# Kernel optimization log

Measured on AMD Instinct MI355X. Metric: run time of the kernel, lower is better.

Reference implementation:

```python
import jax, jax.numpy as jnp
import numpy as np

N = 100000   # num nodes
E = 1200000  # num edges
D = 64       # embedding dim
K = 3        # propagation hops (alpha has K+1 entries)


def setup_inputs() -> dict:
    key = jax.random.key(0)
    k1, k2, k3 = jax.random.split(key, 3)
    edge_index = jax.random.randint(k1, (2, E), 0, N, dtype=jnp.int64)
    weight = jax.random.normal(k2, (N, D), dtype=jnp.float32)
    alpha = jax.random.uniform(k3, (K + 1,), dtype=jnp.float32)
    return {"edge_index": edge_index, "weight": weight, "alpha": alpha}


def reference(edge_index, weight, alpha):
    row = edge_index[0]  # source j
    col = edge_index[1]  # target i
    # symmetric normalization: in-degree over col, deg^-1/2 with inf -> 0
    deg = jax.ops.segment_sum(jnp.ones((E,), dtype=weight.dtype), col, num_segments=N)
    dinv = jnp.where(deg == 0, 0.0, deg ** -0.5)
    edge_w = dinv[row] * dinv[col]  # [E]

    out = weight * alpha[0]
    x = weight
    for k in range(1, K + 1):
        # gather-scale-scatter propagation hop
        msg = edge_w[:, None] * x[row]                      # [E, D]
        x = jax.ops.segment_sum(msg, col, num_segments=N)   # [N, D]
        out = out + x * alpha[k]

    # per-edge link scores: dot(out[src], out[dst])
    return jnp.sum(out[row] * out[col], axis=-1)  # [E]
```

## Files before the change

### kernel.cpp

```cpp
#include <hip/hip_runtime.h>
#include <hip/hip_bf16.h>

#define GN 100000
#define GE 1200000
#define GD 64
#define NG 256
#define CPG 391
#define CAP 6144


__global__ void detect_kernel(const void* __restrict__ w,
                              const void* __restrict__ edge,
                              int* __restrict__ flags, int* __restrict__ gcount) {
    __shared__ int s_badw, s_edgenz;
    if (threadIdx.x == 0) { s_badw = 0; s_edgenz = 0; }
    gcount[threadIdx.x] = 0;
    __syncthreads();
    const unsigned short* wh = (const unsigned short*)w;
    const unsigned int*   ei = (const unsigned int*)edge;
    int badw = 0, edgenz = 0;
    for (int i = threadIdx.x; i < 4096; i += 256) {
        unsigned int bits = ((unsigned int)wh[i]) << 16;
        float v = __uint_as_float(bits);
        if (!(fabsf(v) <= 100.0f)) badw = 1;
        if ((i & 1) == 1 && ei[i] != 0u) edgenz = 1;
    }
    if (badw)   atomicOr(&s_badw, 1);
    if (edgenz) atomicOr(&s_edgenz, 1);
    __syncthreads();
    if (threadIdx.x == 0) {
        flags[0] = s_badw ? 0 : 1;
        flags[1] = s_edgenz ? 0 : 1;
    }
}

__device__ __forceinline__ int ld_row(const int* __restrict__ edge, int e, int e64) {
    return e64 ? edge[2 * (size_t)e] : edge[e];
}
__device__ __forceinline__ int ld_col(const int* __restrict__ edge, int e, int e64) {
    return e64 ? edge[2 * ((size_t)GE + (size_t)e)] : edge[(size_t)GE + (size_t)e];
}
__device__ __forceinline__ float ld_f(const void* __restrict__ p, size_t i, int bf16f) {
    if (bf16f) return __bfloat162float(((const __hip_bfloat16*)p)[i]);
    return ((const float*)p)[i];
}

__device__ __forceinline__ float bf_lo(unsigned u) { return __uint_as_float(u << 16); }
__device__ __forceinline__ float bf_hi(unsigned u) { return __uint_as_float(u & 0xFFFF0000u); }
__device__ __forceinline__ unsigned bf16bits(float f) {
    __hip_bfloat16 h = __float2bfloat16(f);
    unsigned short s;
    __builtin_memcpy(&s, &h, 2);
    return (unsigned)s;
}

__global__ void p1init_kernel(const int* __restrict__ edge, const int* __restrict__ flags,
                              int* __restrict__ gcount, unsigned* __restrict__ bucket,
                              int E, int chunk,
                              const void* __restrict__ w, const void* __restrict__ alpha,
                              __hip_bfloat16* __restrict__ X,
                              __hip_bfloat16* __restrict__ OUT, int nd) {
    if (blockIdx.x < NG) {
        __shared__ int cnt[NG];
        __shared__ int base[NG];
        int t = threadIdx.x;
        int e64 = flags[1];
        cnt[t] = 0;
        __syncthreads();
        int lo = blockIdx.x * chunk;
        int hiE = min(lo + chunk, E);
        for (int e = lo + t; e < hiE; e += 256) {
            int c = ld_col(edge, e, e64);
            int r = ld_row(edge, e, e64);
            if ((unsigned)c < (unsigned)GN && (unsigned)r < (unsigned)GN)
                atomicAdd(&cnt[c / CPG], 1);
        }
        __syncthreads();
        int cv = cnt[t];
        base[t] = (cv > 0) ? atomicAdd(&gcount[t], cv) : 0;
        __syncthreads();
        cnt[t] = 0;
        __syncthreads();
        for (int e = lo + t; e < hiE; e += 256) {
            int c = ld_col(edge, e, e64);
            int r = ld_row(edge, e, e64);
            if ((unsigned)c < (unsigned)GN && (unsigned)r < (unsigned)GN) {
                int g = c / CPG;
                int idx = base[g] + atomicAdd(&cnt[g], 1);
                if (idx < CAP)
                    bucket[(size_t)g * CAP + idx] = ((unsigned)(c - g * CPG) << 17) | (unsigned)r;
            }
        }
    } else {
        int bid = blockIdx.x - NG;
        int i = 4 * (bid * 256 + (int)threadIdx.x);
        int wbf = flags[0];
        if (i < nd) {
            float a0 = ld_f(alpha, 0, wbf);
            float v0 = ld_f(w, i + 0, wbf);
            float v1 = ld_f(w, i + 1, wbf);
            float v2 = ld_f(w, i + 2, wbf);
            float v3 = ld_f(w, i + 3, wbf);
            uint2 xq;
            xq.x = (bf16bits(v1) << 16) | bf16bits(v0);
            xq.y = (bf16bits(v3) << 16) | bf16bits(v2);
            *(uint2*)(X + i) = xq;
            uint2 oq;
            oq.x = (bf16bits(a0 * v1) << 16) | bf16bits(a0 * v0);
            oq.y = (bf16bits(a0 * v3) << 16) | bf16bits(a0 * v2);
            *(uint2*)(OUT + i) = oq;
        }
    }
}

__global__ void p2_kernel(const unsigned* __restrict__ bucket, const int* __restrict__ gcount,
                          int* __restrict__ rowptr, float* __restrict__ dinv,
                          int* __restrict__ csr) {
    int g = blockIdx.x;
    int t = threadIdx.x;
    __shared__ int gs[NG];
    __shared__ int hist[512];
    __shared__ int s[512];
    int gv = gcount[t]; if (gv > CAP) gv = CAP;
    gs[t] = gv;
    hist[t] = 0; hist[t + 256] = 0;
    __syncthreads();
    for (int off = 1; off < NG; off <<= 1) {
        int u = (t >= off) ? gs[t - off] : 0;
        __syncthreads();
        gs[t] += u;
        __syncthreads();
    }
    int mg = gcount[g]; if (mg > CAP) mg = CAP;
    int gb = gs[g] - mg;
    int m = mg;
    const unsigned* bk = bucket + (size_t)g * CAP;
    for (int idx = t; idx < m; idx += 256)
        atomicAdd(&hist[bk[idx] >> 17], 1);
    __syncthreads();
    int h0 = hist[t], h1 = hist[t + 256];
    s[t] = h0; s[t + 256] = h1;
    __syncthreads();
    for (int off = 1; off < 512; off <<= 1) {
        int v0 = (t >= off) ? s[t - off] : 0;
        int v1 = (t + 256 >= off) ? s[t + 256 - off] : 0;
        __syncthreads();
        s[t] += v0; s[t + 256] += v1;
        __syncthreads();
    }
    int col0 = g * CPG + t;
    int col1 = col0 + 256;
    if (col0 < GN) {
        rowptr[col0] = gb + s[t];
        dinv[col0] = (h0 > 0) ? rsqrtf((float)h0) : 0.0f;
    }
    if (t + 256 < CPG && col1 < GN) {
        rowptr[col1] = gb + s[t + 256];
        dinv[col1] = (h1 > 0) ? rsqrtf((float)h1) : 0.0f;
    }
    __syncthreads();
    hist[t] = s[t] - h0;
    hist[t + 256] = s[t + 256] - h1;
    __syncthreads();
    for (int idx = t; idx < m; idx += 256) {
        unsigned u = bk[idx];
        int cl = u >> 17;
        int r  = (int)(u & 0x1FFFFu);
        int pos = gb + atomicAdd(&hist[cl], 1);
        csr[pos] = r;
    }
}

__global__ void gather_kernel(const __hip_bfloat16* __restrict__ X,
                              __hip_bfloat16* __restrict__ Y,
                              __hip_bfloat16* __restrict__ OUT,
                              const int* __restrict__ rowptr, const int* __restrict__ csr,
                              const float* __restrict__ dinv,
                              const void* __restrict__ alpha, const int* __restrict__ flags,
                              int k, int store_y, int N) {
    int t = blockIdx.x * blockDim.x + threadIdx.x;
    int node = __builtin_amdgcn_readfirstlane(t >> 6);
    if (node >= N) return;
    int lane = t & 63;
    int h = lane >> 4;
    int i = lane & 15;
    int beg = node ? rowptr[node - 1] : 0;
    int end = rowptr[node];
    float dc = dinv[node];
    float a = ld_f(alpha, k, flags[0]);
    size_t obase = (size_t)node * GD + 4 * i;
    uint2 uo = *(const uint2*)(OUT + obase);
    float f0 = 0.0f, f1 = 0.0f, f2 = 0.0f, f3 = 0.0f;
    for (int j = beg; j < end; j += 16) {
        int i0 = j + 0 + h;  int i1 = j + 4 + h;
        int i2 = j + 8 + h;  int i3 = j + 12 + h;
        int last = end - 1;
        int r0 = csr[min(i0, last)];
        int r1 = csr[min(i1, last)];
        int r2 = csr[min(i2, last)];
        int r3 = csr[min(i3, last)];
        float w0 = (i0 < end) ? dinv[r0] : 0.0f;
        float w1 = (i1 < end) ? dinv[r1] : 0.0f;
        float w2 = (i2 < end) ? dinv[r2] : 0.0f;
        float w3 = (i3 < end) ? dinv[r3] : 0.0f;
        uint2 u0 = *(const uint2*)(X + (size_t)r0 * GD + 4 * i);
        uint2 u1 = *(const uint2*)(X + (size_t)r1 * GD + 4 * i);
        uint2 u2 = *(const uint2*)(X + (size_t)r2 * GD + 4 * i);
        uint2 u3 = *(const uint2*)(X + (size_t)r3 * GD + 4 * i);
        f0 = fmaf(w0, bf_lo(u0.x), f0); f1 = fmaf(w0, bf_hi(u0.x), f1);
        f2 = fmaf(w0, bf_lo(u0.y), f2); f3 = fmaf(w0, bf_hi(u0.y), f3);
        f0 = fmaf(w1, bf_lo(u1.x), f0); f1 = fmaf(w1, bf_hi(u1.x), f1);
        f2 = fmaf(w1, bf_lo(u1.y), f2); f3 = fmaf(w1, bf_hi(u1.y), f3);
        f0 = fmaf(w2, bf_lo(u2.x), f0); f1 = fmaf(w2, bf_hi(u2.x), f1);
        f2 = fmaf(w2, bf_lo(u2.y), f2); f3 = fmaf(w2, bf_hi(u2.y), f3);
        f0 = fmaf(w3, bf_lo(u3.x), f0); f1 = fmaf(w3, bf_hi(u3.x), f1);
        f2 = fmaf(w3, bf_lo(u3.y), f2); f3 = fmaf(w3, bf_hi(u3.y), f3);
    }
    f0 += __shfl_xor(f0, 16, 64); f0 += __shfl_xor(f0, 32, 64);
    f1 += __shfl_xor(f1, 16, 64); f1 += __shfl_xor(f1, 32, 64);
    f2 += __shfl_xor(f2, 16, 64); f2 += __shfl_xor(f2, 32, 64);
    f3 += __shfl_xor(f3, 16, 64); f3 += __shfl_xor(f3, 32, 64);
    f0 *= dc; f1 *= dc; f2 *= dc; f3 *= dc;
    if (h == 0) {
        if (store_y) {
            uint2 p;
            p.x = (bf16bits(f1) << 16) | bf16bits(f0);
            p.y = (bf16bits(f3) << 16) | bf16bits(f2);
            *(uint2*)(Y + obase) = p;
        }
        float o0 = fmaf(a, f0, bf_lo(uo.x));
        float o1 = fmaf(a, f1, bf_hi(uo.x));
        float o2 = fmaf(a, f2, bf_lo(uo.y));
        float o3 = fmaf(a, f3, bf_hi(uo.y));
        uint2 q;
        q.x = (bf16bits(o1) << 16) | bf16bits(o0);
        q.y = (bf16bits(o3) << 16) | bf16bits(o2);
        *(uint2*)(OUT + obase) = q;
    }
}

__device__ __forceinline__ float dot2_bf16(unsigned ua, unsigned ub) {
    return fmaf(bf_lo(ua), bf_lo(ub), bf_hi(ua) * bf_hi(ub));
}

__global__ void dot_kernel(const __hip_bfloat16* __restrict__ OUT,
                           const int* __restrict__ edge, const int* __restrict__ flags,
                           void* __restrict__ res, int E) {
    int t = blockIdx.x * blockDim.x + threadIdx.x;
    int e = t >> 2;
    int sub = t & 3;
    if (e >= E) return;
    int e64 = flags[1];
    int wbf = flags[0];
    int r = ld_row(edge, e, e64);
    int c = ld_col(edge, e, e64);
    float p = 0.0f;
    if ((unsigned)r < (unsigned)GN && (unsigned)c < (unsigned)GN) {
        const uint4* pa = (const uint4*)(OUT + (size_t)r * GD + sub * 16);
        const uint4* pb = (const uint4*)(OUT + (size_t)c * GD + sub * 16);
        uint4 a0 = pa[0], a1 = pa[1];
        uint4 b0 = pb[0], b1 = pb[1];
        p = ((dot2_bf16(a0.x, b0.x) + dot2_bf16(a0.y, b0.y)) +
             (dot2_bf16(a0.z, b0.z) + dot2_bf16(a0.w, b0.w))) +
            ((dot2_bf16(a1.x, b1.x) + dot2_bf16(a1.y, b1.y)) +
             (dot2_bf16(a1.z, b1.z) + dot2_bf16(a1.w, b1.w)));
    }
    p += __shfl_down(p, 2, 4);
    p += __shfl_down(p, 1, 4);
    if (sub == 0) {
        if (wbf) ((__hip_bfloat16*)res)[e] = __float2bfloat16(p);
        else     ((float*)res)[e] = p;
    }
}

extern "C" void kernel_launch(void* const* d_in, const int* in_sizes, int n_in,
                              void* d_out, int out_size, void* d_ws, size_t ws_size,
                              hipStream_t stream) {
    const int E = GE, N = GN, ND = GN * GD;

    const void* edge   = d_in[0];
    const void* weight = d_in[1];
    const void* alpha  = d_in[2];

    char* ws = (char*)d_ws;
    int*      flags     = (int*)ws;      ws += 256;
    int*      gcount    = (int*)ws;      ws += 1024;
    float*    dinv      = (float*)ws;    ws += (((size_t)N * 4 + 255) / 256) * 256;
    int*      rowptr    = (int*)ws;      ws += (((size_t)N * 4 + 255) / 256) * 256;
    unsigned* bucket    = (unsigned*)ws; ws += (size_t)NG * CAP * 4;
    int*      csr       = (int*)ws;      ws += (size_t)E * 4;
    __hip_bfloat16* X   = (__hip_bfloat16*)ws; ws += (size_t)ND * 2;
    __hip_bfloat16* Y   = (__hip_bfloat16*)ws; ws += (size_t)ND * 2;
    __hip_bfloat16* OUT = (__hip_bfloat16*)ws; ws += (size_t)ND * 2;

    const int B = 256;

    detect_kernel<<<1, 256, 0, stream>>>(weight, edge, flags, gcount);

    {
        const int chunk = (E + NG - 1) / NG;
        const int initBlocks = (ND / 4 + B - 1) / B;
        p1init_kernel<<<NG + initBlocks, B, 0, stream>>>(
            (const int*)edge, flags, gcount, bucket, E, chunk,
            weight, alpha, X, OUT, ND);
    }
    p2_kernel<<<NG, 256, 0, stream>>>(bucket, gcount, rowptr, dinv, csr);

    const int ggrid = (int)(((size_t)N * 64 + B - 1) / B);
    gather_kernel<<<ggrid, B, 0, stream>>>(X, Y, OUT, rowptr, csr, dinv, alpha, flags, 1, 1, N);
    gather_kernel<<<ggrid, B, 0, stream>>>(Y, X, OUT, rowptr, csr, dinv, alpha, flags, 2, 1, N);
    gather_kernel<<<ggrid, B, 0, stream>>>(X, Y, OUT, rowptr, csr, dinv, alpha, flags, 3, 0, N);

    dot_kernel<<<(int)(((size_t)E * 4 + B - 1) / B), B, 0, stream>>>(OUT, (const int*)edge, flags, d_out, E);
}
```

Before: 275.2 us.

## Fuse three gather hops and edge dot into one cooperative persistent kernel

Replaces the three per-hop gather launches and the dot-product launch with a single cooperative kernel. Persistent waves loop over nodes and edges, and each phase is separated by a grid-wide barrier. This is meant to remove launch gaps and tail effects between kernels, at the cost of grid.sync overhead and occupancy capped by the co-residency requirement. The grid size comes from an occupancy query that assumes 256 compute units.

```diff
diff --git a/kernel.cpp b/kernel.cpp
--- a/kernel.cpp
+++ b/kernel.cpp
@@ -1,5 +1,8 @@
 #include <hip/hip_runtime.h>
 #include <hip/hip_bf16.h>
+#include <hip/hip_cooperative_groups.h>
+
+namespace cg = cooperative_groups;
 
 #define GN 100000
 #define GE 1200000
@@ -171,23 +174,17 @@
     }
 }
 
-__global__ void gather_kernel(const __hip_bfloat16* __restrict__ X,
-                              __hip_bfloat16* __restrict__ Y,
-                              __hip_bfloat16* __restrict__ OUT,
-                              const int* __restrict__ rowptr, const int* __restrict__ csr,
-                              const float* __restrict__ dinv,
-                              const void* __restrict__ alpha, const int* __restrict__ flags,
-                              int k, int store_y, int N) {
-    int t = blockIdx.x * blockDim.x + threadIdx.x;
-    int node = __builtin_amdgcn_readfirstlane(t >> 6);
-    if (node >= N) return;
-    int lane = t & 63;
+__device__ __forceinline__ void gather_node(
+        const __hip_bfloat16* __restrict__ X, __hip_bfloat16* __restrict__ Y,
+        __hip_bfloat16* __restrict__ OUT,
+        const int* __restrict__ rowptr, const int* __restrict__ csr,
+        const float* __restrict__ dinv, float a, int store_y,
+        int node, int lane) {
     int h = lane >> 4;
     int i = lane & 15;
     int beg = node ? rowptr[node - 1] : 0;
     int end = rowptr[node];
     float dc = dinv[node];
-    float a = ld_f(alpha, k, flags[0]);
     size_t obase = (size_t)node * GD + 4 * i;
     uint2 uo = *(const uint2*)(OUT + obase);
     float f0 = 0.0f, f1 = 0.0f, f2 = 0.0f, f3 = 0.0f;
@@ -243,33 +240,69 @@
     return fmaf(bf_lo(ua), bf_lo(ub), bf_hi(ua) * bf_hi(ub));
 }
 
-__global__ void dot_kernel(const __hip_bfloat16* __restrict__ OUT,
-                           const int* __restrict__ edge, const int* __restrict__ flags,
-                           void* __restrict__ res, int E) {
-    int t = blockIdx.x * blockDim.x + threadIdx.x;
-    int e = t >> 2;
-    int sub = t & 3;
-    if (e >= E) return;
+__global__ void coop_kernel(__hip_bfloat16* __restrict__ X,
+                            __hip_bfloat16* __restrict__ Y,
+                            __hip_bfloat16* __restrict__ OUT,
+                            const int* __restrict__ rowptr, const int* __restrict__ csr,
+                            const float* __restrict__ dinv,
+                            const void* __restrict__ alpha, const int* __restrict__ flags,
+                            const int* __restrict__ edge, void* __restrict__ res,
+                            int N, int E) {
+    cg::grid_group grid = cg::this_grid();
+    int lane = threadIdx.x & 63;
+    int wslot = blockIdx.x * 4 + (threadIdx.x >> 6);
+    int totalWaves = gridDim.x * 4;
+    int wbf = flags[0];
     int e64 = flags[1];
-    int wbf = flags[0];
-    int r = ld_row(edge, e, e64);
-    int c = ld_col(edge, e, e64);
-    float p = 0.0f;
-    if ((unsigned)r < (unsigned)GN && (unsigned)c < (unsigned)GN) {
-        const uint4* pa = (const uint4*)(OUT + (size_t)r * GD + sub * 16);
-        const uint4* pb = (const uint4*)(OUT + (size_t)c * GD + sub * 16);
-        uint4 a0 = pa[0], a1 = pa[1];
-        uint4 b0 = pb[0], b1 = pb[1];
-        p = ((dot2_bf16(a0.x, b0.x) + dot2_bf16(a0.y, b0.y)) +
-             (dot2_bf16(a0.z, b0.z) + dot2_bf16(a0.w, b0.w))) +
-            ((dot2_bf16(a1.x, b1.x) + dot2_bf16(a1.y, b1.y)) +
-             (dot2_bf16(a1.z, b1.z) + dot2_bf16(a1.w, b1.w)));
-    }
-    p += __shfl_down(p, 2, 4);
-    p += __shfl_down(p, 1, 4);
-    if (sub == 0) {
-        if (wbf) ((__hip_bfloat16*)res)[e] = __float2bfloat16(p);
-        else     ((float*)res)[e] = p;
+
+    {
+        float a = ld_f(alpha, 1, wbf);
+        for (int node = wslot; node < N; node += totalWaves)
+            gather_node(X, Y, OUT, rowptr, csr, dinv, a, 1, node, lane);
+    }
+    __threadfence();
+    grid.sync();
+    {
+        float a = ld_f(alpha, 2, wbf);
+        for (int node = wslot; node < N; node += totalWaves)
+            gather_node(Y, X, OUT, rowptr, csr, dinv, a, 1, node, lane);
+    }
+    __threadfence();
+    grid.sync();
+    {
+        float a = ld_f(alpha, 3, wbf);
+        for (int node = wslot; node < N; node += totalWaves)
+            gather_node(X, Y, OUT, rowptr, csr, dinv, a, 0, node, lane);
+    }
+    __threadfence();
+    grid.sync();
+    {
+        int tid = blockIdx.x * 256 + threadIdx.x;
+        int tot = gridDim.x * 256;
+        long long totalT = (long long)E * 4;
+        for (long long t4 = tid; t4 < totalT; t4 += tot) {
+            int e = (int)(t4 >> 2);
+            int sub = (int)(t4 & 3);
+            int r = ld_row(edge, e, e64);
+            int c = ld_col(edge, e, e64);
+            float p = 0.0f;
+            if ((unsigned)r < (unsigned)GN && (unsigned)c < (unsigned)GN) {
+                const uint4* pa = (const uint4*)(OUT + (size_t)r * GD + sub * 16);
+                const uint4* pb = (const uint4*)(OUT + (size_t)c * GD + sub * 16);
+                uint4 a0 = pa[0], a1 = pa[1];
+                uint4 b0 = pb[0], b1 = pb[1];
+                p = ((dot2_bf16(a0.x, b0.x) + dot2_bf16(a0.y, b0.y)) +
+                     (dot2_bf16(a0.z, b0.z) + dot2_bf16(a0.w, b0.w))) +
+                    ((dot2_bf16(a1.x, b1.x) + dot2_bf16(a1.y, b1.y)) +
+                     (dot2_bf16(a1.z, b1.z) + dot2_bf16(a1.w, b1.w)));
+            }
+            p += __shfl_down(p, 2, 4);
+            p += __shfl_down(p, 1, 4);
+            if (sub == 0) {
+                if (wbf) ((__hip_bfloat16*)res)[e] = __float2bfloat16(p);
+                else     ((float*)res)[e] = p;
+            }
+        }
     }
 }
 
@@ -306,10 +339,20 @@
     }
     p2_kernel<<<NG, 256, 0, stream>>>(bucket, gcount, rowptr, dinv, csr);
 
-    const int ggrid = (int)(((size_t)N * 64 + B - 1) / B);
-    gather_kernel<<<ggrid, B, 0, stream>>>(X, Y, OUT, rowptr, csr, dinv, alpha, flags, 1, 1, N);
-    gather_kernel<<<ggrid, B, 0, stream>>>(Y, X, OUT, rowptr, csr, dinv, alpha, flags, 2, 1, N);
-    gather_kernel<<<ggrid, B, 0, stream>>>(X, Y, OUT, rowptr, csr, dinv, alpha, flags, 3, 0, N);
-
-    dot_kernel<<<(int)(((size_t)E * 4 + B - 1) / B), B, 0, stream>>>(OUT, (const int*)edge, flags, d_out, E);
-}
+    {
+        int maxB = 0;
+        hipOccupancyMaxActiveBlocksPerMultiprocessor(&maxB, coop_kernel, 256, 0);
+        if (maxB < 1) maxB = 4;
+        int grid = maxB * 256;
+        if (grid > 25000) grid = 25000;
+
+        __hip_bfloat16* Xa = X; __hip_bfloat16* Ya = Y; __hip_bfloat16* Oa = OUT;
+        const int* rp = rowptr; const int* cs = csr; const float* dv = dinv;
+        const void* al = alpha; const int* fl = flags;
+        const int* ed = (const int*)edge; void* rs = d_out;
+        int Na = N, Ea = E;
+        void* args[] = { &Xa, &Ya, &Oa, &rp, &cs, &dv, &al, &fl, &ed, &rs, &Na, &Ea };
+        hipLaunchCooperativeKernel((void*)coop_kernel, dim3(grid), dim3(B),
+                                   args, 0, stream);
+    }
+}
```

After: 990.3 us. +259.8%, slower.
